# Optimization experiments

Hardware: AMD Instinct MI355X
Metric: run time of the kernel (lower is better)

The kernel has to match this reference:

```python
import jax, jax.numpy as jnp
import numpy as np

NEG_INF = -1e30  # value the original assigns to exactly-zero scores


def setup_inputs() -> dict:
    key = jax.random.key(0)
    kq, kk, kv = jax.random.split(key, 3)
    B, Lq, Lk, d = 16, 4096, 4096, 64
    queries = jax.random.normal(kq, (B, Lq, d), dtype=jnp.float32)
    keys = jax.random.normal(kk, (B, Lk, d), dtype=jnp.float32)
    values = jax.random.normal(kv, (B, Lk, d), dtype=jnp.float32)
    return {"queries": queries, "keys": keys, "values": values}


def reference(queries, keys, values):
    d = queries.shape[-1]
    # [B, Lq, Lk] full score matrix, scaled
    scores = jnp.einsum("bqd,bkd->bqk", queries, keys) / jnp.sqrt(
        jnp.asarray(d, dtype=queries.dtype)
    )
    # zero-score masking: scores[scores == 0] = -1e30
    scores = jnp.where(scores == 0, jnp.asarray(NEG_INF, dtype=scores.dtype), scores)
    attn = jax.nn.softmax(scores, axis=-1)
    # dropout prob is 0.0 -> identity
    return jnp.einsum("bqk,bkd->bqd", attn, values)
```

## Files before the change

### kernel.cpp

```cpp
#include <hip/hip_runtime.h>
#include <hip/hip_bf16.h>
#include <math.h>

typedef __attribute__((ext_vector_type(4))) float f32x4;
typedef __attribute__((ext_vector_type(8))) short s16x8;

#define B_    16
#define L_    4096
#define D_    64
#define QB    128
#define KVB   64
#define NT    (L_ / KVB)

#define QSCALE 0.18033688011112042f
#define THR    8.0f

__device__ __forceinline__ unsigned short f2bf(float x) {
  union { float f; unsigned u; } v; v.f = x;
  unsigned r = v.u + 0x7FFFu + ((v.u >> 16) & 1u);
  return (unsigned short)(r >> 16);
}

__device__ __forceinline__ int swz(int x) {
  return ((x & 7) ^ ((x >> 3) & 7)) << 4;
}

__device__ __forceinline__ void gload_lds16(const void* g, void* l) {
  __builtin_amdgcn_global_load_lds(
      (const __attribute__((address_space(1))) void*)g,
      (__attribute__((address_space(3))) void*)l, 16, 0, 0);
}

__device__ __forceinline__ unsigned cvtpk_bf16(float lo, float hi) {
  unsigned r;
  asm("v_cvt_pk_bf16_f32 %0, %1, %2" : "=v"(r) : "v"(lo), "v"(hi));
  return r;
}

__device__ __forceinline__ void pl32_swap(unsigned& a, unsigned& b) {
#if __has_builtin(__builtin_amdgcn_permlane32_swap)
  auto r = __builtin_amdgcn_permlane32_swap(a, b, false, false);
  a = r[0]; b = r[1];
#else
  asm volatile("v_permlane32_swap_b32 %0, %1" : "+v"(a), "+v"(b));
#endif
}

__device__ __forceinline__ void pl16_swap(unsigned& a, unsigned& b) {
#if __has_builtin(__builtin_amdgcn_permlane16_swap)
  auto r = __builtin_amdgcn_permlane16_swap(a, b, false, false);
  a = r[0]; b = r[1];
#else
  asm volatile("v_permlane16_swap_b32 %0, %1" : "+v"(a), "+v"(b));
#endif
}

__device__ __forceinline__ float fexp2(float x) {
#if __has_builtin(__builtin_amdgcn_exp2f)
  return __builtin_amdgcn_exp2f(x);
#else
  return exp2f(x);
#endif
}

__global__ __launch_bounds__(256) void prep_kv4(
    const float* __restrict__ Kg, const float* __restrict__ Vg,
    unsigned short* __restrict__ Kw, unsigned short* __restrict__ Vw) {
  __shared__ unsigned short vim[KVB * D_];
  const int tid = threadIdx.x;
  int blk = blockIdx.x;
  if (blk < B_ * NT) {
    const float* src = Kg + (size_t)blk * (KVB * D_);
    char* dst = (char*)(Kw + (size_t)blk * (KVB * D_));
#pragma unroll
    for (int c = 0; c < 2; ++c) {
      const int ch  = tid + c * 256;
      const int key = ch >> 3;
      const int seg = ch & 7;
      const float* p = src + key * D_ + seg * 8;
      f32x4 x0 = *(const f32x4*)p;
      f32x4 x1 = *(const f32x4*)(p + 4);
      union { s16x8 v; unsigned w[4]; } t_;
      t_.w[0] = cvtpk_bf16(x0[0], x0[1]);
      t_.w[1] = cvtpk_bf16(x0[2], x0[3]);
      t_.w[2] = cvtpk_bf16(x1[0], x1[1]);
      t_.w[3] = cvtpk_bf16(x1[2], x1[3]);
      *(s16x8*)(dst + ((key * 128 + seg * 16) ^ swz(key))) = t_.v;
    }
  } else {
    blk -= B_ * NT;
    const int skey2 = (tid >> 3) * 2;
    const int sdseg = tid & 7;
    const float* vp0 = Vg + ((size_t)blk * KVB + skey2) * D_ + sdseg * 8;
    char* vimc = (char*)vim;
    f32x4 v0 = *(const f32x4*)(vp0);
    f32x4 v1 = *(const f32x4*)(vp0 + 4);
    f32x4 v2 = *(const f32x4*)(vp0 + D_);
    f32x4 v3 = *(const f32x4*)(vp0 + D_ + 4);
#pragma unroll
    for (int u = 0; u < 2; ++u) {
#pragma unroll
      for (int i = 0; i < 4; ++i) {
        const int d = sdseg * 8 + u * 4 + i;
        unsigned pk = cvtpk_bf16(u ? v1[i] : v0[i], u ? v3[i] : v2[i]);
        *(unsigned*)(vimc + ((d * 128 + skey2 * 2) ^ swz(d))) = pk;
      }
    }
    __syncthreads();
    char* vout = (char*)(Vw + (size_t)blk * (KVB * D_));
#pragma unroll
    for (int c = 0; c < 2; ++c) {
      const int off = c * 4096 + tid * 16;
      *(s16x8*)(vout + off) = *(const s16x8*)(vimc + off);
    }
  }
}

__global__ __launch_bounds__(256, 2) void attn_fwd6(
    const float* __restrict__ Qg, const unsigned short* __restrict__ Kw,
    const unsigned short* __restrict__ Vw, float* __restrict__ Og) {
  __shared__ unsigned short Ks[4][KVB * D_];
  __shared__ unsigned short Vs[4][KVB * D_];

  const int tid  = threadIdx.x;
  const int wv   = tid >> 6;
  const int lane = tid & 63;
  const int rl   = lane & 15;
  const int kb   = lane >> 4;
  const int kb4  = kb * 4;

  const int blk = blockIdx.x;
  const int b   = blk >> 5;
  const int qt  = blk & 31;

  const float* qbase = Qg + ((size_t)b * L_ + qt * QB + wv * 32) * D_;
  s16x8 aq0[2], aq1[2];
#pragma unroll
  for (int qh = 0; qh < 2; ++qh) {
    const float* qrow_p = qbase + (qh * 16 + rl) * D_;
#pragma unroll
    for (int h = 0; h < 2; ++h) {
      const float* p = qrow_p + h * 32 + kb * 8;
      f32x4 x0 = *(const f32x4*)p;
      f32x4 x1 = *(const f32x4*)(p + 4);
      union { s16x8 v; unsigned w[4]; } t_;
      t_.w[0] = cvtpk_bf16(x0[0] * QSCALE, x0[1] * QSCALE);
      t_.w[1] = cvtpk_bf16(x0[2] * QSCALE, x0[3] * QSCALE);
      t_.w[2] = cvtpk_bf16(x1[0] * QSCALE, x1[1] * QSCALE);
      t_.w[3] = cvtpk_bf16(x1[2] * QSCALE, x1[3] * QSCALE);
      if (qh == 0) aq0[h] = t_.v; else aq1[h] = t_.v;
    }
  }

  int offA[4], offB[4];
#pragma unroll
  for (int t = 0; t < 4; ++t) {
    const int row  = t * 16 + rl;
    const int base = row * 128 + kb * 16;
    offA[t] = base ^ swz(row);
    offB[t] = (base + 64) ^ swz(row);
  }

  f32x4 oacc0[4], oacc1[4];
#pragma unroll
  for (int t = 0; t < 4; ++t) {
    oacc0[t] = (f32x4){0.f, 0.f, 0.f, 0.f};
    oacc1[t] = (f32x4){0.f, 0.f, 0.f, 0.f};
  }
  float m0 = -3.0e38f, m1 = -3.0e38f, l0 = 0.f, l1 = 0.f;

  char* ks0 = (char*)(&Ks[0][0]);
  char* vs0 = (char*)(&Vs[0][0]);
  const int woff = wv * 2048;
  const char* kt = (const char*)(Kw + (size_t)b * L_ * D_) + woff + lane * 16;
  const char* vt = (const char*)(Vw + (size_t)b * L_ * D_) + woff + lane * 16;

  auto issue = [&](int bi) {
    char* kd = ks0 + bi * 8192 + woff;
    char* vd = vs0 + bi * 8192 + woff;
    gload_lds16(kt,        kd);
    gload_lds16(kt + 1024, kd + 1024);
    gload_lds16(vt,        vd);
    gload_lds16(vt + 1024, vd + 1024);
    kt += 8192; vt += 8192;
  };

  auto compute = [&](const char* kbase, const char* vbase) {
    f32x4 s0[4], s1[4];
    __builtin_amdgcn_s_setprio(1);
#pragma unroll
    for (int t = 0; t < 4; ++t) {
      s16x8 k0 = *(const s16x8*)(kbase + offA[t]);
      s16x8 k1 = *(const s16x8*)(kbase + offB[t]);
      f32x4 a = (f32x4){0.f, 0.f, 0.f, 0.f};
      f32x4 c = (f32x4){0.f, 0.f, 0.f, 0.f};
      a = __builtin_amdgcn_mfma_f32_16x16x32_bf16(k0, aq0[0], a, 0, 0, 0);
      c = __builtin_amdgcn_mfma_f32_16x16x32_bf16(k0, aq1[0], c, 0, 0, 0);
      a = __builtin_amdgcn_mfma_f32_16x16x32_bf16(k1, aq0[1], a, 0, 0, 0);
      c = __builtin_amdgcn_mfma_f32_16x16x32_bf16(k1, aq1[1], c, 0, 0, 0);
      s0[t] = a; s1[t] = c;
    }
    __builtin_amdgcn_s_setprio(0);

    float x0 = fmaxf(fmaxf(s0[0][0], s0[0][1]), fmaxf(s0[0][2], s0[0][3]));
    float x1 = fmaxf(fmaxf(s0[1][0], s0[1][1]), fmaxf(s0[1][2], s0[1][3]));
    float x2 = fmaxf(fmaxf(s0[2][0], s0[2][1]), fmaxf(s0[2][2], s0[2][3]));
    float x3 = fmaxf(fmaxf(s0[3][0], s0[3][1]), fmaxf(s0[3][2], s0[3][3]));
    float mx0 = fmaxf(fmaxf(x0, x1), fmaxf(x2, x3));
    float y0 = fmaxf(fmaxf(s1[0][0], s1[0][1]), fmaxf(s1[0][2], s1[0][3]));
    float y1 = fmaxf(fmaxf(s1[1][0], s1[1][1]), fmaxf(s1[1][2], s1[1][3]));
    float y2 = fmaxf(fmaxf(s1[2][0], s1[2][1]), fmaxf(s1[2][2], s1[2][3]));
    float y3 = fmaxf(fmaxf(s1[3][0], s1[3][1]), fmaxf(s1[3][2], s1[3][3]));
    float mx1 = fmaxf(fmaxf(y0, y1), fmaxf(y2, y3));

    if (__any((mx0 > m0 + THR) || (mx1 > m1 + THR))) {
      float r0 = fmaxf(mx0, __shfl_xor(mx0, 16));
      r0 = fmaxf(r0, __shfl_xor(r0, 32));
      float r1 = fmaxf(mx1, __shfl_xor(mx1, 16));
      r1 = fmaxf(r1, __shfl_xor(r1, 32));
      const float n0 = fmaxf(m0, r0);
      const float n1 = fmaxf(m1, r1);
      const float al0 = fexp2(m0 - n0);
      const float al1 = fexp2(m1 - n1);
      m0 = n0; m1 = n1;
      l0 *= al0; l1 *= al1;
#pragma unroll
      for (int j = 0; j < 4; ++j) {
        const float b0 = __shfl(al0, kb4 + j);
        const float b1 = __shfl(al1, kb4 + j);
#pragma unroll
        for (int t = 0; t < 4; ++t) {
          oacc0[t][j] *= b0;
          oacc1[t][j] *= b1;
        }
      }
    }

    unsigned W0[4][2], W1[4][2];
    float rs0 = 0.f, rs1 = 0.f;
#pragma unroll
    for (int t = 0; t < 4; ++t) {
      const float e0 = fexp2(s0[t][0] - m0);
      const float e1 = fexp2(s0[t][1] - m0);
      const float e2 = fexp2(s0[t][2] - m0);
      const float e3 = fexp2(s0[t][3] - m0);
      rs0 += (e0 + e1) + (e2 + e3);
      W0[t][0] = cvtpk_bf16(e0, e1);
      W0[t][1] = cvtpk_bf16(e2, e3);
      const float f0 = fexp2(s1[t][0] - m1);
      const float f1 = fexp2(s1[t][1] - m1);
      const float f2 = fexp2(s1[t][2] - m1);
      const float f3 = fexp2(s1[t][3] - m1);
      rs1 += (f0 + f1) + (f2 + f3);
      W1[t][0] = cvtpk_bf16(f0, f1);
      W1[t][1] = cvtpk_bf16(f2, f3);
    }
    l0 += rs0; l1 += rs1;

    union { s16x8 v; unsigned w[4]; } A00, A01, A10, A11;
#pragma unroll
    for (int u = 0; u < 2; ++u) {
      { unsigned x = W0[0][u], y = W0[1][u];
        pl32_swap(x, y); pl16_swap(x, y);
        A00.w[u] = x; A00.w[u + 2] = y; }
      { unsigned x = W0[2][u], y = W0[3][u];
        pl32_swap(x, y); pl16_swap(x, y);
        A01.w[u] = x; A01.w[u + 2] = y; }
      { unsigned x = W1[0][u], y = W1[1][u];
        pl32_swap(x, y); pl16_swap(x, y);
        A10.w[u] = x; A10.w[u + 2] = y; }
      { unsigned x = W1[2][u], y = W1[3][u];
        pl32_swap(x, y); pl16_swap(x, y);
        A11.w[u] = x; A11.w[u + 2] = y; }
    }

    __builtin_amdgcn_s_setprio(1);
#pragma unroll
    for (int t = 0; t < 4; ++t) {
      s16x8 bv0 = *(const s16x8*)(vbase + offA[t]);
      s16x8 bv1 = *(const s16x8*)(vbase + offB[t]);
      f32x4 a = oacc0[t];
      f32x4 c = oacc1[t];
      a = __builtin_amdgcn_mfma_f32_16x16x32_bf16(A00.v, bv0, a, 0, 0, 0);
      c = __builtin_amdgcn_mfma_f32_16x16x32_bf16(A10.v, bv0, c, 0, 0, 0);
      a = __builtin_amdgcn_mfma_f32_16x16x32_bf16(A01.v, bv1, a, 0, 0, 0);
      c = __builtin_amdgcn_mfma_f32_16x16x32_bf16(A11.v, bv1, c, 0, 0, 0);
      oacc0[t] = a; oacc1[t] = c;
    }
    __builtin_amdgcn_s_setprio(0);
  };

  issue(0); issue(1); issue(2);

  for (int i = 0; i < NT - 3; ++i) {
    asm volatile("s_waitcnt vmcnt(8)" ::: "memory");
    __builtin_amdgcn_sched_barrier(0);
    __builtin_amdgcn_s_barrier();
    __builtin_amdgcn_sched_barrier(0);
    issue((i + 3) & 3);
    compute(ks0 + (i & 3) * 8192, vs0 + (i & 3) * 8192);
  }

  asm volatile("s_waitcnt vmcnt(8)" ::: "memory");
  __builtin_amdgcn_sched_barrier(0);
  __builtin_amdgcn_s_barrier();
  __builtin_amdgcn_sched_barrier(0);
  compute(ks0 + ((NT - 3) & 3) * 8192, vs0 + ((NT - 3) & 3) * 8192);

  asm volatile("s_waitcnt vmcnt(4)" ::: "memory");
  __builtin_amdgcn_sched_barrier(0);
  __builtin_amdgcn_s_barrier();
  __builtin_amdgcn_sched_barrier(0);
  compute(ks0 + ((NT - 2) & 3) * 8192, vs0 + ((NT - 2) & 3) * 8192);

  asm volatile("s_waitcnt vmcnt(0)" ::: "memory");
  __builtin_amdgcn_sched_barrier(0);
  __builtin_amdgcn_s_barrier();
  __builtin_amdgcn_sched_barrier(0);
  compute(ks0 + ((NT - 1) & 3) * 8192, vs0 + ((NT - 1) & 3) * 8192);

  float t0 = l0 + __shfl_xor(l0, 16);
  t0 += __shfl_xor(t0, 32);
  float t1 = l1 + __shfl_xor(l1, 16);
  t1 += __shfl_xor(t1, 32);
  const float v0i = 1.0f / t0;
  const float v1i = 1.0f / t1;

  float* ob = Og + ((size_t)b * L_ + qt * QB + wv * 32 + kb4) * D_;
#pragma unroll
  for (int j = 0; j < 4; ++j) {
    const float i0 = __shfl(v0i, kb4 + j);
    const float i1 = __shfl(v1i, kb4 + j);
    float* r0 = ob + (size_t)j * D_;
    float* r1 = r0 + 16 * D_;
#pragma unroll
    for (int t = 0; t < 4; ++t) {
      r0[t * 16 + rl] = oacc0[t][j] * i0;
      r1[t * 16 + rl] = oacc1[t][j] * i1;
    }
  }
}

__global__ __launch_bounds__(256) void attn_fwd_fb(
    const float* __restrict__ Qg, const float* __restrict__ Kg,
    const float* __restrict__ Vg, float* __restrict__ Og) {
  __shared__ unsigned short Ksf[KVB * D_];
  __shared__ unsigned short Vsf[KVB * D_];
  __shared__ unsigned short Psf[4][16 * KVB];

  const int tid  = threadIdx.x;
  const int wv   = tid >> 6;
  const int lane = tid & 63;
  const int rl   = lane & 15;
  const int kb   = lane >> 4;

  const int blk = blockIdx.x;
  const int b   = blk / (L_ / 64);
  const int qt  = blk % (L_ / 64);

  const float* qrow_p = Qg + ((size_t)b * L_ + qt * 64 + wv * 16 + rl) * D_;
  s16x8 aq[2];
#pragma unroll
  for (int h = 0; h < 2; ++h) {
    const float* p = qrow_p + h * 32 + kb * 8;
    f32x4 x0 = *(const f32x4*)p;
    f32x4 x1 = *(const f32x4*)(p + 4);
    s16x8 w;
#pragma unroll
    for (int i = 0; i < 4; ++i) {
      w[i]     = (short)f2bf(x0[i] * QSCALE);
      w[i + 4] = (short)f2bf(x1[i] * QSCALE);
    }
    aq[h] = w;
  }

  f32x4 oacc[4];
  float m_r[4], l_r[4];
#pragma unroll
  for (int t = 0; t < 4; ++t) oacc[t] = (f32x4){0.f, 0.f, 0.f, 0.f};
#pragma unroll
  for (int j = 0; j < 4; ++j) { m_r[j] = -3.0e38f; l_r[j] = 0.f; }

  const float* kb_p = Kg + (size_t)b * L_ * D_;
  const float* vb_p = Vg + (size_t)b * L_ * D_;
  const int skey2 = (tid >> 3) * 2;
  const int sdseg = tid & 7;

  char* ksc = (char*)Ksf;
  char* vsc = (char*)Vsf;
  char* psc = (char*)(Psf[wv]);

  for (int kv = 0; kv < L_; kv += KVB) {
    __syncthreads();
    {
      const float* kp0 = kb_p + (size_t)(kv + skey2) * D_ + sdseg * 8;
      const float* vp0 = vb_p + (size_t)(kv + skey2) * D_ + sdseg * 8;
#pragma unroll
      for (int q2 = 0; q2 < 2; ++q2) {
        const int key = skey2 + q2;
        f32x4 a0 = *(const f32x4*)(kp0 + q2 * D_);
        f32x4 a1 = *(const f32x4*)(kp0 + q2 * D_ + 4);
        s16x8 w;
#pragma unroll
        for (int i = 0; i < 4; ++i) {
          w[i]     = (short)f2bf(a0[i]);
          w[i + 4] = (short)f2bf(a1[i]);
        }
        *(s16x8*)(ksc + ((key * 128 + sdseg * 16) ^ swz(key))) = w;
      }
      f32x4 v0 = *(const f32x4*)(vp0);
      f32x4 v1 = *(const f32x4*)(vp0 + 4);
      f32x4 v2 = *(const f32x4*)(vp0 + D_);
      f32x4 v3 = *(const f32x4*)(vp0 + D_ + 4);
#pragma unroll
      for (int u = 0; u < 2; ++u) {
#pragma unroll
        for (int i = 0; i < 4; ++i) {
          const int d = sdseg * 8 + u * 4 + i;
          unsigned lo = (unsigned)f2bf(u ? v1[i] : v0[i]);
          unsigned hi = (unsigned)f2bf(u ? v3[i] : v2[i]);
          *(unsigned*)(vsc + ((d * 128 + skey2 * 2) ^ swz(d))) = lo | (hi << 16);
        }
      }
    }
    __syncthreads();

    f32x4 s[4];
#pragma unroll
    for (int t = 0; t < 4; ++t) {
      const int key  = t * 16 + rl;
      const int base = key * 128 + kb * 16;
      s16x8 b0 = *(const s16x8*)(ksc + ((base)      ^ swz(key)));
      s16x8 b1 = *(const s16x8*)(ksc + ((base + 64) ^ swz(key)));
      f32x4 acc = (f32x4){0.f, 0.f, 0.f, 0.f};
      acc = __builtin_amdgcn_mfma_f32_16x16x32_bf16(aq[0], b0, acc, 0, 0, 0);
      acc = __builtin_amdgcn_mfma_f32_16x16x32_bf16(aq[1], b1, acc, 0, 0, 0);
      s[t] = acc;
    }

    float alpha[4];
#pragma unroll
    for (int j = 0; j < 4; ++j) {
      float mx = fmaxf(fmaxf(s[0][j], s[1][j]), fmaxf(s[2][j], s[3][j]));
      mx = fmaxf(mx, __shfl_xor(mx, 1));
      mx = fmaxf(mx, __shfl_xor(mx, 2));
      mx = fmaxf(mx, __shfl_xor(mx, 4));
      mx = fmaxf(mx, __shfl_xor(mx, 8));
      const float mn = fmaxf(m_r[j], mx);
      alpha[j] = fexp2(m_r[j] - mn);
      m_r[j]   = mn;
    }

    float rs[4] = {0.f, 0.f, 0.f, 0.f};
#pragma unroll
    for (int t = 0; t < 4; ++t)
#pragma unroll
      for (int j = 0; j < 4; ++j) {
        const float p = fexp2(s[t][j] - m_r[j]);
        rs[j] += p;
        const int row = kb * 4 + j;
        *(unsigned short*)(psc + ((row * 128 + (t * 16 + rl) * 2) ^ swz(row))) = f2bf(p);
      }
#pragma unroll
    for (int j = 0; j < 4; ++j) l_r[j] = l_r[j] * alpha[j] + rs[j];

#pragma unroll
    for (int t = 0; t < 4; ++t)
#pragma unroll
      for (int j = 0; j < 4; ++j) oacc[t][j] *= alpha[j];

    s16x8 ap[2];
#pragma unroll
    for (int h = 0; h < 2; ++h) {
      const int base = rl * 128 + h * 64 + kb * 16;
      ap[h] = *(const s16x8*)(psc + (base ^ swz(rl)));
    }
#pragma unroll
    for (int t = 0; t < 4; ++t) {
      const int d    = t * 16 + rl;
      const int base = d * 128 + kb * 16;
      s16x8 bv0 = *(const s16x8*)(vsc + ((base)      ^ swz(d)));
      s16x8 bv1 = *(const s16x8*)(vsc + ((base + 64) ^ swz(d)));
      f32x4 acc = oacc[t];
      acc = __builtin_amdgcn_mfma_f32_16x16x32_bf16(ap[0], bv0, acc, 0, 0, 0);
      acc = __builtin_amdgcn_mfma_f32_16x16x32_bf16(ap[1], bv1, acc, 0, 0, 0);
      oacc[t] = acc;
    }
  }

  float inv[4];
#pragma unroll
  for (int j = 0; j < 4; ++j) {
    float r = l_r[j];
    r += __shfl_xor(r, 1);
    r += __shfl_xor(r, 2);
    r += __shfl_xor(r, 4);
    r += __shfl_xor(r, 8);
    inv[j] = 1.0f / r;
  }
  float* op = Og + ((size_t)b * L_ + qt * 64 + wv * 16 + kb * 4) * D_;
#pragma unroll
  for (int j = 0; j < 4; ++j)
#pragma unroll
    for (int t = 0; t < 4; ++t)
      op[(size_t)j * D_ + t * 16 + rl] = oacc[t][j] * inv[j];
}

extern "C" void kernel_launch(void* const* d_in, const int* in_sizes, int n_in,
                              void* d_out, int out_size, void* d_ws, size_t ws_size,
                              hipStream_t stream) {
  (void)in_sizes; (void)n_in; (void)out_size;
  const float* Q = (const float*)d_in[0];
  const float* K = (const float*)d_in[1];
  const float* V = (const float*)d_in[2];
  float* O = (float*)d_out;

  const size_t need = (size_t)2 * B_ * L_ * D_ * sizeof(unsigned short);
  if (d_ws != nullptr && ws_size >= need) {
    unsigned short* Kw = (unsigned short*)d_ws;
    unsigned short* Vw = Kw + (size_t)B_ * L_ * D_;
    prep_kv4<<<dim3(2 * B_ * NT), 256, 0, stream>>>(K, V, Kw, Vw);
    attn_fwd6<<<dim3(B_ * (L_ / QB)), 256, 0, stream>>>(Q, Kw, Vw, O);
  } else {
    attn_fwd_fb<<<dim3(B_ * (L_ / 64)), 256, 0, stream>>>(Q, K, V, O);
  }
}
```

Measured before the change: 191.1 us.

## Use five-stage KV ring and process two tiles per barrier

Grows the shared-memory K/V ring from four to five stages and restructures the main loop so each barrier covers two KV tiles: it issues two async loads, then computes two tiles. This halves the number of workgroup barriers and waits per tile. The setprio bracketing also moves out of the inner compute phases so priority spans both tile computations. LDS use rises to 80KB per block, which may still allow two blocks per CU but leaves less headroom.

```diff
diff --git a/kernel.cpp b/kernel.cpp
--- a/kernel.cpp
+++ b/kernel.cpp
@@ -116,11 +116,11 @@
   }
 }
 
-__global__ __launch_bounds__(256, 2) void attn_fwd6(
+__global__ __launch_bounds__(256, 2) void attn_fwd7(
     const float* __restrict__ Qg, const unsigned short* __restrict__ Kw,
     const unsigned short* __restrict__ Vw, float* __restrict__ Og) {
-  __shared__ unsigned short Ks[4][KVB * D_];
-  __shared__ unsigned short Vs[4][KVB * D_];
+  __shared__ unsigned short Ks[5][KVB * D_];
+  __shared__ unsigned short Vs[5][KVB * D_];
 
   const int tid  = threadIdx.x;
   const int wv   = tid >> 6;
@@ -171,23 +171,24 @@
 
   char* ks0 = (char*)(&Ks[0][0]);
   char* vs0 = (char*)(&Vs[0][0]);
-  const int woff = wv * 2048;
-  const char* kt = (const char*)(Kw + (size_t)b * L_ * D_) + woff + lane * 16;
-  const char* vt = (const char*)(Vw + (size_t)b * L_ * D_) + woff + lane * 16;
-
-  auto issue = [&](int bi) {
+  const int woff   = wv * 2048;
+  const int lane16 = lane * 16;
+  const char* kimg = (const char*)(Kw + (size_t)b * L_ * D_) + woff + lane16;
+  const char* vimg = (const char*)(Vw + (size_t)b * L_ * D_) + woff + lane16;
+
+  auto issue = [&](int s, int bi) {
+    const char* kg = kimg + (size_t)s * 8192;
+    const char* vg = vimg + (size_t)s * 8192;
     char* kd = ks0 + bi * 8192 + woff;
     char* vd = vs0 + bi * 8192 + woff;
-    gload_lds16(kt,        kd);
-    gload_lds16(kt + 1024, kd + 1024);
-    gload_lds16(vt,        vd);
-    gload_lds16(vt + 1024, vd + 1024);
-    kt += 8192; vt += 8192;
+    gload_lds16(kg,        kd);
+    gload_lds16(kg + 1024, kd + 1024);
+    gload_lds16(vg,        vd);
+    gload_lds16(vg + 1024, vd + 1024);
   };
 
   auto compute = [&](const char* kbase, const char* vbase) {
     f32x4 s0[4], s1[4];
-    __builtin_amdgcn_s_setprio(1);
 #pragma unroll
     for (int t = 0; t < 4; ++t) {
       s16x8 k0 = *(const s16x8*)(kbase + offA[t]);
@@ -200,7 +201,6 @@
       c = __builtin_amdgcn_mfma_f32_16x16x32_bf16(k1, aq1[1], c, 0, 0, 0);
       s0[t] = a; s1[t] = c;
     }
-    __builtin_amdgcn_s_setprio(0);
 
     float x0 = fmaxf(fmaxf(s0[0][0], s0[0][1]), fmaxf(s0[0][2], s0[0][3]));
     float x1 = fmaxf(fmaxf(s0[1][0], s0[1][1]), fmaxf(s0[1][2], s0[1][3]));
@@ -274,7 +274,6 @@
         A11.w[u] = x; A11.w[u + 2] = y; }
     }
 
-    __builtin_amdgcn_s_setprio(1);
 #pragma unroll
     for (int t = 0; t < 4; ++t) {
       s16x8 bv0 = *(const s16x8*)(vbase + offA[t]);
@@ -287,37 +286,49 @@
       c = __builtin_amdgcn_mfma_f32_16x16x32_bf16(A11.v, bv1, c, 0, 0, 0);
       oacc0[t] = a; oacc1[t] = c;
     }
-    __builtin_amdgcn_s_setprio(0);
   };
 
-  issue(0); issue(1); issue(2);
-
-  for (int i = 0; i < NT - 3; ++i) {
-    asm volatile("s_waitcnt vmcnt(8)" ::: "memory");
+  issue(0, 0); issue(1, 1); issue(2, 2);
+
+  int c0 = 0, c1 = 1, b3 = 3, b4 = 4;
+  for (int p = 0; p < 30; ++p) {
+    const int i = 2 * p;
+    asm volatile("s_waitcnt vmcnt(4)" ::: "memory");
     __builtin_amdgcn_sched_barrier(0);
     __builtin_amdgcn_s_barrier();
     __builtin_amdgcn_sched_barrier(0);
-    issue((i + 3) & 3);
-    compute(ks0 + (i & 3) * 8192, vs0 + (i & 3) * 8192);
-  }
-
-  asm volatile("s_waitcnt vmcnt(8)" ::: "memory");
-  __builtin_amdgcn_sched_barrier(0);
-  __builtin_amdgcn_s_barrier();
-  __builtin_amdgcn_sched_barrier(0);
-  compute(ks0 + ((NT - 3) & 3) * 8192, vs0 + ((NT - 3) & 3) * 8192);
+    issue(i + 3, b3);
+    issue(i + 4, b4);
+    __builtin_amdgcn_s_setprio(1);
+    compute(ks0 + c0 * 8192, vs0 + c0 * 8192);
+    compute(ks0 + c1 * 8192, vs0 + c1 * 8192);
+    __builtin_amdgcn_s_setprio(0);
+    c0 += 2; if (c0 >= 5) c0 -= 5;
+    c1 += 2; if (c1 >= 5) c1 -= 5;
+    b3 += 2; if (b3 >= 5) b3 -= 5;
+    b4 += 2; if (b4 >= 5) b4 -= 5;
+  }
 
   asm volatile("s_waitcnt vmcnt(4)" ::: "memory");
   __builtin_amdgcn_sched_barrier(0);
   __builtin_amdgcn_s_barrier();
   __builtin_amdgcn_sched_barrier(0);
-  compute(ks0 + ((NT - 2) & 3) * 8192, vs0 + ((NT - 2) & 3) * 8192);
+  issue(63, b3);
+  __builtin_amdgcn_s_setprio(1);
+  compute(ks0 + c0 * 8192, vs0 + c0 * 8192);
+  compute(ks0 + c1 * 8192, vs0 + c1 * 8192);
+  __builtin_amdgcn_s_setprio(0);
+  c0 += 2; if (c0 >= 5) c0 -= 5;
+  c1 += 2; if (c1 >= 5) c1 -= 5;
 
   asm volatile("s_waitcnt vmcnt(0)" ::: "memory");
   __builtin_amdgcn_sched_barrier(0);
   __builtin_amdgcn_s_barrier();
   __builtin_amdgcn_sched_barrier(0);
-  compute(ks0 + ((NT - 1) & 3) * 8192, vs0 + ((NT - 1) & 3) * 8192);
+  __builtin_amdgcn_s_setprio(1);
+  compute(ks0 + c0 * 8192, vs0 + c0 * 8192);
+  compute(ks0 + c1 * 8192, vs0 + c1 * 8192);
+  __builtin_amdgcn_s_setprio(0);
 
   float t0 = l0 + __shfl_xor(l0, 16);
   t0 += __shfl_xor(t0, 32);
@@ -520,7 +531,7 @@
     unsigned short* Kw = (unsigned short*)d_ws;
     unsigned short* Vw = Kw + (size_t)B_ * L_ * D_;
     prep_kv4<<<dim3(2 * B_ * NT), 256, 0, stream>>>(K, V, Kw, Vw);
-    attn_fwd6<<<dim3(B_ * (L_ / QB)), 256, 0, stream>>>(Q, Kw, Vw, O);
+    attn_fwd7<<<dim3(B_ * (L_ / QB)), 256, 0, stream>>>(Q, Kw, Vw, O);
   } else {
     attn_fwd_fb<<<dim3(B_ * (L_ / 64)), 256, 0, stream>>>(Q, K, V, O);
   }
```

Measured after the change: 189.2 us. Within noise of the previous version (-1.0%).
